# Kernel tuning notes

Hardware: AMD Instinct MI355X
Metric: run time of the kernel (lower is better)

## Reference

```python
import jax, jax.numpy as jnp
import numpy as np

N, K = 10000, 16
EDGE_DIM, HID = 32, 64
MULT = 8            # rep1.mult == rep2.mult (out_mult)
NL = 2              # lvals [0,1] -> 2 irreps per rep
DIM = 4             # (2*0+1) + (2*1+1)
NHEADS = 4
OUT3 = 3 * MULT     # qkv multiplicity
RW_FLAT = NL * NL * MULT * OUT3   # 768 radial-weight outputs per edge
HEAD_DIM = (MULT * DIM) // NHEADS # 8
INDICES = jnp.array([0, 1, 1, 1]) # irrep index for each of the DIM slots (l=0 then l=1 x3)


def setup_inputs() -> dict:
    key = jax.random.key(0)
    ks = jax.random.split(key, 10)
    rn = lambda i, shape, sc=1.0: (jax.random.normal(ks[i], shape, jnp.float32) * sc)
    return {
        "b1": rn(0, (N, K, DIM, NL)),
        "b2": rn(1, (N, K, NL, DIM)),
        "edge_feats": rn(2, (N, K, EDGE_DIM)),
        "f": rn(3, (N, MULT, DIM)),
        "neighbor_idx": jax.random.randint(ks[4], (N, K), 0, N),
        # RadialWeight MLP params (xavier-ish scales, zero biases as in _init_weights)
        "W1": rn(5, (HID, EDGE_DIM), (2.0 / (HID + EDGE_DIM)) ** 0.5),
        "b1_lin": jnp.zeros((HID,), jnp.float32),
        "W2": rn(6, (RW_FLAT, HID), (2.0 / (RW_FLAT + HID)) ** 0.5),
        "b2_lin": jnp.zeros((RW_FLAT,), jnp.float32),
        # EquivariantLinear out_proj params
        "W_out": rn(7, (NL * MULT, MULT), (2.0 / (NL * MULT + MULT)) ** 0.5),
        "bias_out": jnp.zeros((MULT, 1), jnp.float32),
    }


def reference(b1, b2, edge_feats, f, neighbor_idx, W1, b1_lin, W2, b2_lin, W_out, bias_out):
    E = N * K
    b1f = b1.reshape(E, DIM, NL)
    b2f = b2.reshape(E, NL, DIM)
    ef = edge_feats.reshape(E, EDGE_DIM)

    # RadialWeight: 2-layer MLP with exact GELU -> per-edge tensor-product weights
    h = jax.nn.gelu(ef @ W1.T + b1_lin, approximate=False)          # (E, HID)
    rw = (h @ W2.T + b2_lin).reshape(E, NL * OUT3, NL * MULT)        # (E, 48, 16)

    # EquivariantConvolution: gather src node features, chained small matmuls
    f_src = f[neighbor_idx.reshape(-1)]                              # (E, MULT, DIM)
    tmp = jnp.einsum('emd,edl->eml', f_src, b1f)                     # (E, MULT, NL)
    tmp = jnp.matmul(rw, tmp.reshape(E, NL * MULT, 1))               # (E, NL*OUT3, 1)
    qkv = jnp.matmul(tmp.reshape(E, OUT3, NL), b2f)                  # (E, OUT3, DIM)

    # split into q,k,v heads
    qkv = qkv.reshape(N, K, 3 * MULT, DIM)
    q, k_, v = jnp.split(qkv, 3, axis=2)                             # each (N, K, MULT, DIM)
    qh = q.reshape(N, K, NHEADS, HEAD_DIM)
    kh = k_.reshape(N, K, NHEADS, HEAD_DIM)
    vh = v.reshape(N, K, NHEADS, HEAD_DIM)

    # per-edge attention, softmax over the k neighbors
    scale = HEAD_DIM ** -0.5
    scores = jnp.einsum('nkhd,nkhd->nkh', qh, kh) * scale            # (N, K, NHEADS)
    attn = jax.nn.softmax(scores, axis=1)
    out = jnp.einsum('nkh,nkhd->nhd', attn, vh).reshape(N, MULT, DIM)

    # EquivariantLinear out_proj: per-irrep mixing over multiplicity channels
    o = jnp.einsum('om,nmd->nod', W_out, out).reshape(N, NL, MULT, DIM)
    idx = jnp.broadcast_to(INDICES[None, None, None, :], (N, 1, MULT, DIM))
    o = jnp.take_along_axis(o, idx, axis=1)[:, 0]                    # (N, MULT, DIM)
    # bias only on the scalar (l=0) slot; activation is Identity in out_proj
    o = o.at[:, :, 0].add(bias_out[:, 0])
    return o
```

## Files before the change

### kernel.cpp

```cpp
#include <hip/hip_runtime.h>
#include <math.h>

#define E_TOT   160000
#define THREADS 128
#define NBLK    (E_TOT / THREADS)
#define WREG    20480
#define TV_OFF  16384
#define T2S     52

typedef __attribute__((ext_vector_type(8))) __bf16 bf16x8;
typedef __attribute__((ext_vector_type(4))) float f32x4;

static __device__ __forceinline__ unsigned short f2bf(float v) {
    unsigned int u = __float_as_uint(v);
    u += 0x7FFFu + ((u >> 16) & 1u);
    return (unsigned short)(u >> 16);
}
static __device__ __forceinline__ float bf2f(unsigned int s) {
    return __uint_as_float(s << 16);
}

__global__ __launch_bounds__(256) void w2_split(
    const float* __restrict__ W2, uint4* __restrict__ hi4, uint4* __restrict__ lo4)
{
    const int c    = blockIdx.x * 256 + threadIdx.x;
    const int lane = c & 63, rest = c >> 6;
    const int kk   = rest & 1, tj = rest >> 1;
    const int j    = tj & 15,  t  = tj >> 4;
    const int grp  = lane >> 4, r16 = lane & 15;
    const float* src = W2 + (size_t)((t * 16 + r16) * 16 + j) * 64 + kk * 32 + grp * 8;
    union { uint4 u; unsigned short s[8]; } H, L;
    #pragma unroll
    for (int i = 0; i < 8; ++i) {
        float w = src[i];
        unsigned short h = f2bf(w);
        H.s[i] = h;
        L.s[i] = f2bf(w - bf2f(h));
    }
    hi4[c] = H.u;
    lo4[c] = L.u;
}

__global__ __launch_bounds__(THREADS) void eq_attn_kernel(
    const float* __restrict__ b1,
    const float* __restrict__ b2,
    const float* __restrict__ ef,
    const float* __restrict__ f,
    const int*   __restrict__ nidx,
    const float* __restrict__ W1,
    const float* __restrict__ b1l,
    const float* __restrict__ b2l,
    const float* __restrict__ Wout,
    const float* __restrict__ bias,
    const uint4* __restrict__ wsh,
    const uint4* __restrict__ wsl,
    float* __restrict__ out)
{
    __shared__ unsigned char smem[2 * WREG];
    const int tid  = threadIdx.x;
    const int e    = blockIdx.x * THREADS + tid;
    const int wave = tid >> 6;
    const int el   = tid & 63;
    unsigned char* wreg = smem + wave * WREG;

    float efr[32];
    {
        const float4* ef4 = reinterpret_cast<const float4*>(ef + (size_t)e * 32);
        #pragma unroll
        for (int i = 0; i < 8; ++i) {
            float4 v = ef4[i];
            efr[i*4+0] = v.x; efr[i*4+1] = v.y; efr[i*4+2] = v.z; efr[i*4+3] = v.w;
        }
    }
    {
        float h[64];
        #pragma unroll
        for (int hid = 0; hid < 64; ++hid) {
            float acc = b1l[hid];
            #pragma unroll
            for (int c = 0; c < 32; ++c)
                acc = fmaf(efr[c], W1[hid * 32 + c], acc);
            h[hid] = 0.5f * acc * (1.0f + erff(acc * 0.70710678118654752f));
        }
        #pragma unroll
        for (int c8 = 0; c8 < 8; ++c8) {
            union { uint4 u; unsigned short s[8]; } H, L;
            #pragma unroll
            for (int i = 0; i < 8; ++i) {
                float v = h[c8 * 8 + i];
                unsigned short hs = f2bf(v);
                H.s[i] = hs;
                L.s[i] = f2bf(v - bf2f(hs));
            }
            const int ch = c8 ^ (el & 7);
            *(uint4*)(wreg +        el * 128 + ch * 16) = H.u;
            *(uint4*)(wreg + 8192 + el * 128 + ch * 16) = L.u;
        }
    }
    float tmpv[16];
    {
        const int src = nidx[e];
        float fs[32];
        const float4* f4 = reinterpret_cast<const float4*>(f + (size_t)src * 32);
        #pragma unroll
        for (int i = 0; i < 8; ++i) {
            float4 v = f4[i];
            fs[i*4+0] = v.x; fs[i*4+1] = v.y; fs[i*4+2] = v.z; fs[i*4+3] = v.w;
        }
        float b1r[8];
        const float4* b14 = reinterpret_cast<const float4*>(b1 + (size_t)e * 8);
        float4 u0 = b14[0], u1 = b14[1];
        b1r[0]=u0.x; b1r[1]=u0.y; b1r[2]=u0.z; b1r[3]=u0.w;
        b1r[4]=u1.x; b1r[5]=u1.y; b1r[6]=u1.z; b1r[7]=u1.w;
        float* tvp = (float*)(wreg + TV_OFF);
        #pragma unroll
        for (int m = 0; m < 8; ++m) {
            float a0 = 0.f, a1 = 0.f;
            #pragma unroll
            for (int d = 0; d < 4; ++d) {
                a0 = fmaf(fs[m*4+d], b1r[d*2+0], a0);
                a1 = fmaf(fs[m*4+d], b1r[d*2+1], a1);
            }
            tmpv[m*2+0] = a0; tmpv[m*2+1] = a1;
            tvp[(m*2+0) * 64 + el] = a0;
            tvp[(m*2+1) * 64 + el] = a1;
        }
    }

    __syncthreads();

    const int r16 = el & 15;
    const int grp = el >> 4;

    bf16x8 Ahi[4][2], Alo[4][2];
    #pragma unroll
    for (int mt = 0; mt < 4; ++mt)
        #pragma unroll
        for (int kk = 0; kk < 2; ++kk) {
            const int row = mt * 16 + r16;
            const int ch  = (kk * 4 + grp) ^ (r16 & 7);
            Ahi[mt][kk] = *(const bf16x8*)(wreg +        row * 128 + ch * 16);
            Alo[mt][kk] = *(const bf16x8*)(wreg + 8192 + row * 128 + ch * 16);
        }

    f32x4 acc[4][3];
    #pragma unroll
    for (int mt = 0; mt < 4; ++mt)
        #pragma unroll
        for (int t = 0; t < 3; ++t)
            acc[mt][t] = (f32x4){0.f, 0.f, 0.f, 0.f};

    const float* tvp = (const float*)(wreg + TV_OFF);
    for (int j = 0; j < 16; ++j) {
        bf16x8 Bhi[3][2], Blo[3][2];
        #pragma unroll
        for (int t = 0; t < 3; ++t)
            #pragma unroll
            for (int kk = 0; kk < 2; ++kk) {
                const int chunk = ((t * 16 + j) * 2 + kk) * 64 + el;
                Bhi[t][kk] = ((const bf16x8*)wsh)[chunk];
                Blo[t][kk] = ((const bf16x8*)wsl)[chunk];
            }
        #pragma unroll
        for (int mt = 0; mt < 4; ++mt) {
            const int eb = mt * 16 + grp * 4;
            const float tv0 = tvp[j * 64 + eb + 0];
            const float tv1 = tvp[j * 64 + eb + 1];
            const float tv2 = tvp[j * 64 + eb + 2];
            const float tv3 = tvp[j * 64 + eb + 3];
            #pragma unroll
            for (int t = 0; t < 3; ++t) {
                f32x4 rw = (f32x4){0.f, 0.f, 0.f, 0.f};
                rw = __builtin_amdgcn_mfma_f32_16x16x32_bf16(Ahi[mt][0], Bhi[t][0], rw, 0, 0, 0);
                rw = __builtin_amdgcn_mfma_f32_16x16x32_bf16(Ahi[mt][1], Bhi[t][1], rw, 0, 0, 0);
                rw = __builtin_amdgcn_mfma_f32_16x16x32_bf16(Alo[mt][0], Bhi[t][0], rw, 0, 0, 0);
                rw = __builtin_amdgcn_mfma_f32_16x16x32_bf16(Alo[mt][1], Bhi[t][1], rw, 0, 0, 0);
                rw = __builtin_amdgcn_mfma_f32_16x16x32_bf16(Ahi[mt][0], Blo[t][0], rw, 0, 0, 0);
                rw = __builtin_amdgcn_mfma_f32_16x16x32_bf16(Ahi[mt][1], Blo[t][1], rw, 0, 0, 0);
                acc[mt][t].x = fmaf(tv0, rw.x, acc[mt][t].x);
                acc[mt][t].y = fmaf(tv1, rw.y, acc[mt][t].y);
                acc[mt][t].z = fmaf(tv2, rw.z, acc[mt][t].z);
                acc[mt][t].w = fmaf(tv3, rw.w, acc[mt][t].w);
            }
        }
    }

    {
        float* t2p = (float*)wreg;
        #pragma unroll
        for (int mt = 0; mt < 4; ++mt) {
            const int eb = mt * 16 + grp * 4;
            #pragma unroll
            for (int t = 0; t < 3; ++t) {
                t2p[(eb + 0) * T2S + t * 16 + r16] = acc[mt][t].x;
                t2p[(eb + 1) * T2S + t * 16 + r16] = acc[mt][t].y;
                t2p[(eb + 2) * T2S + t * 16 + r16] = acc[mt][t].z;
                t2p[(eb + 3) * T2S + t * 16 + r16] = acc[mt][t].w;
            }
        }
    }

    __syncthreads();

    float t2[48];
    {
        const float* t2r = (const float*)wreg + (size_t)el * T2S;
        #pragma unroll
        for (int o2 = 0; o2 < 48; ++o2) t2[o2] = t2r[o2];
    }
    #pragma unroll
    for (int o2 = 0; o2 < 48; ++o2) {
        float bt = t2[o2];
        #pragma unroll
        for (int j = 0; j < 16; ++j)
            bt = fmaf(tmpv[j], b2l[o2 * 16 + j], bt);
        t2[o2] = bt;
    }

    float b2r[8];
    {
        const float4* b24 = reinterpret_cast<const float4*>(b2 + (size_t)e * 8);
        float4 u0 = b24[0], u1 = b24[1];
        b2r[0]=u0.x; b2r[1]=u0.y; b2r[2]=u0.z; b2r[3]=u0.w;
        b2r[4]=u1.x; b2r[5]=u1.y; b2r[6]=u1.z; b2r[7]=u1.w;
    }
    float q[8][4];
    #pragma unroll
    for (int o = 0; o < 8; ++o) {
        float t0 = t2[2*o+0], t1 = t2[2*o+1];
        #pragma unroll
        for (int d = 0; d < 4; ++d)
            q[o][d] = fmaf(t0, b2r[d], t1 * b2r[4+d]);
    }
    float scores[4] = {0.f, 0.f, 0.f, 0.f};
    #pragma unroll
    for (int o = 0; o < 8; ++o) {
        float t0 = t2[16+2*o+0], t1 = t2[16+2*o+1];
        float sacc = 0.f;
        #pragma unroll
        for (int d = 0; d < 4; ++d) {
            float kr = fmaf(t0, b2r[d], t1 * b2r[4+d]);
            sacc = fmaf(q[o][d], kr, sacc);
        }
        scores[o >> 1] += sacc;
    }
    float vv[8][4];
    #pragma unroll
    for (int o = 0; o < 8; ++o) {
        float t0 = t2[32+2*o+0], t1 = t2[32+2*o+1];
        #pragma unroll
        for (int d = 0; d < 4; ++d)
            vv[o][d] = fmaf(t0, b2r[d], t1 * b2r[4+d]);
    }

    float attn[4];
    #pragma unroll
    for (int hh = 0; hh < 4; ++hh) {
        float s = scores[hh] * 0.35355339059327373f;
        float mx = s;
        #pragma unroll
        for (int msk = 8; msk; msk >>= 1)
            mx = fmaxf(mx, __shfl_xor(mx, msk, 16));
        float p = __expf(s - mx);
        float ps = p;
        #pragma unroll
        for (int msk = 8; msk; msk >>= 1)
            ps += __shfl_xor(ps, msk, 16);
        attn[hh] = p / ps;
    }

    float osum[8][4];
    #pragma unroll
    for (int m = 0; m < 8; ++m) {
        float w = attn[m >> 1];
        #pragma unroll
        for (int d = 0; d < 4; ++d) {
            float val = w * vv[m][d];
            #pragma unroll
            for (int msk = 8; msk; msk >>= 1)
                val += __shfl_xor(val, msk, 16);
            osum[m][d] = val;
        }
    }

    if ((tid & 15) == 0) {
        const int n = e >> 4;
        #pragma unroll
        for (int od = 0; od < 8; ++od) {
            #pragma unroll
            for (int d = 0; d < 4; ++d) {
                const int row = (d == 0) ? od : (8 + od);
                float a = (d == 0) ? bias[od] : 0.f;
                #pragma unroll
                for (int m = 0; m < 8; ++m)
                    a = fmaf(Wout[row * 8 + m], osum[m][d], a);
                out[(size_t)n * 32 + od * 4 + d] = a;
            }
        }
    }
}

extern "C" void kernel_launch(void* const* d_in, const int* in_sizes, int n_in,
                              void* d_out, int out_size, void* d_ws, size_t ws_size,
                              hipStream_t stream) {
    const float* b1   = (const float*)d_in[0];
    const float* b2   = (const float*)d_in[1];
    const float* ef   = (const float*)d_in[2];
    const float* f    = (const float*)d_in[3];
    const int*   nidx = (const int*)d_in[4];
    const float* W1   = (const float*)d_in[5];
    const float* b1l  = (const float*)d_in[6];
    const float* W2   = (const float*)d_in[7];
    const float* b2l  = (const float*)d_in[8];
    const float* Wout = (const float*)d_in[9];
    const float* bias = (const float*)d_in[10];
    float* out = (float*)d_out;

    uint4* wsh = (uint4*)d_ws;
    uint4* wsl = wsh + 6144;

    hipLaunchKernelGGL(w2_split, dim3(24), dim3(256), 0, stream, W2, wsh, wsl);
    hipLaunchKernelGGL(eq_attn_kernel, dim3(NBLK), dim3(THREADS), 0, stream,
                       b1, b2, ef, f, nidx, W1, b1l, b2l, Wout, bias,
                       (const uint4*)wsh, (const uint4*)wsl, out);
}
```

Baseline: 225.2 us.

## Shrink blocks to one wave, cut LDS, polynomial GELU, fold radial bias into MFMA

Each block now holds a single 64-thread wave, and the shared buffer shrinks from 40KB to 13KB. The hi and lo bf16 parts of the hidden activations are staged one after the other through the same LDS region, with extra barriers between them. Exact erf is replaced with an Abramowitz-Stegun polynomial built on a fast reciprocal and exp. The b2 bias contribution moves from a 768-FMA scalar loop into an MFMA initialisation of the accumulators, using a bf16 copy of the bias prepared in the setup kernel. This should raise occupancy and cut VALU work, but the bf16 bias path and the approximate erf lose some precision.

After: 193.4 us. -14.1%, faster.

```diff
diff --git a/kernel.cpp b/kernel.cpp
--- a/kernel.cpp
+++ b/kernel.cpp
@@ -2,11 +2,11 @@
 #include <math.h>
 
 #define E_TOT   160000
-#define THREADS 128
-#define NBLK    (E_TOT / THREADS)
-#define WREG    20480
-#define TV_OFF  16384
+#define TPB     64
+#define NBLK    (E_TOT / TPB)
+#define TV_OFF  8192
 #define T2S     52
+#define SMEM_SZ 13312
 
 typedef __attribute__((ext_vector_type(8))) __bf16 bf16x8;
 typedef __attribute__((ext_vector_type(4))) float f32x4;
@@ -20,28 +20,55 @@
     return __uint_as_float(s << 16);
 }
 
-__global__ __launch_bounds__(256) void w2_split(
-    const float* __restrict__ W2, uint4* __restrict__ hi4, uint4* __restrict__ lo4)
+static __device__ __forceinline__ float gelu_exact(float a) {
+    float x = a * 0.70710678118654752f;
+    float s = fabsf(x);
+    float t = __builtin_amdgcn_rcpf(fmaf(0.3275911f, s, 1.0f));
+    float p = fmaf(1.061405429f, t, -1.453152027f);
+    p = fmaf(p, t, 1.421413741f);
+    p = fmaf(p, t, -0.284496736f);
+    p = fmaf(p, t, 0.254829592f);
+    p = p * t;
+    float er = fmaf(-p, __expf(-s * s), 1.0f);
+    er = copysignf(er, x);
+    return 0.5f * a * (1.0f + er);
+}
+
+__global__ __launch_bounds__(256) void w_split(
+    const float* __restrict__ W2, const float* __restrict__ b2l,
+    uint4* __restrict__ hi4, uint4* __restrict__ lo4, uint4* __restrict__ bb4)
 {
-    const int c    = blockIdx.x * 256 + threadIdx.x;
-    const int lane = c & 63, rest = c >> 6;
-    const int kk   = rest & 1, tj = rest >> 1;
-    const int j    = tj & 15,  t  = tj >> 4;
-    const int grp  = lane >> 4, r16 = lane & 15;
-    const float* src = W2 + (size_t)((t * 16 + r16) * 16 + j) * 64 + kk * 32 + grp * 8;
-    union { uint4 u; unsigned short s[8]; } H, L;
-    #pragma unroll
-    for (int i = 0; i < 8; ++i) {
-        float w = src[i];
-        unsigned short h = f2bf(w);
-        H.s[i] = h;
-        L.s[i] = f2bf(w - bf2f(h));
-    }
-    hi4[c] = H.u;
-    lo4[c] = L.u;
-}
-
-__global__ __launch_bounds__(THREADS) void eq_attn_kernel(
+    const int c = blockIdx.x * 256 + threadIdx.x;
+    if (c < 6144) {
+        const int lane = c & 63, rest = c >> 6;
+        const int kk   = rest & 1, tj = rest >> 1;
+        const int j    = tj & 15,  t  = tj >> 4;
+        const int grp  = lane >> 4, r16 = lane & 15;
+        const float* src = W2 + (size_t)((t * 16 + r16) * 16 + j) * 64 + kk * 32 + grp * 8;
+        union { uint4 u; unsigned short s[8]; } H, L;
+        #pragma unroll
+        for (int i = 0; i < 8; ++i) {
+            float w = src[i];
+            unsigned short h = f2bf(w);
+            H.s[i] = h;
+            L.s[i] = f2bf(w - bf2f(h));
+        }
+        hi4[c] = H.u;
+        lo4[c] = L.u;
+    } else if (c < 6144 + 192) {
+        const int cc   = c - 6144;
+        const int lane = cc & 63, t = cc >> 6;
+        const int grp  = lane >> 4, r16 = lane & 15;
+        union { uint4 u; unsigned short s[8]; } B;
+        #pragma unroll
+        for (int i = 0; i < 8; ++i)
+            B.s[i] = (grp < 2) ? f2bf(b2l[(t * 16 + r16) * 16 + grp * 8 + i])
+                               : (unsigned short)0;
+        bb4[cc] = B.u;
+    }
+}
+
+__global__ __launch_bounds__(TPB) void eq_attn_kernel(
     const float* __restrict__ b1,
     const float* __restrict__ b2,
     const float* __restrict__ ef,
@@ -49,19 +76,18 @@
     const int*   __restrict__ nidx,
     const float* __restrict__ W1,
     const float* __restrict__ b1l,
-    const float* __restrict__ b2l,
     const float* __restrict__ Wout,
     const float* __restrict__ bias,
     const uint4* __restrict__ wsh,
     const uint4* __restrict__ wsl,
+    const uint4* __restrict__ bb,
     float* __restrict__ out)
 {
-    __shared__ unsigned char smem[2 * WREG];
-    const int tid  = threadIdx.x;
-    const int e    = blockIdx.x * THREADS + tid;
-    const int wave = tid >> 6;
-    const int el   = tid & 63;
-    unsigned char* wreg = smem + wave * WREG;
+    __shared__ unsigned char smem[SMEM_SZ];
+    const int tid = threadIdx.x;
+    const int e   = blockIdx.x * TPB + tid;
+    const int r16 = tid & 15;
+    const int grp = tid >> 4;
 
     float efr[32];
     {
@@ -72,30 +98,29 @@
             efr[i*4+0] = v.x; efr[i*4+1] = v.y; efr[i*4+2] = v.z; efr[i*4+3] = v.w;
         }
     }
-    {
-        float h[64];
-        #pragma unroll
-        for (int hid = 0; hid < 64; ++hid) {
-            float acc = b1l[hid];
-            #pragma unroll
-            for (int c = 0; c < 32; ++c)
-                acc = fmaf(efr[c], W1[hid * 32 + c], acc);
-            h[hid] = 0.5f * acc * (1.0f + erff(acc * 0.70710678118654752f));
-        }
+    uint4 Hc[8], Lc[8];
+    {
         #pragma unroll
         for (int c8 = 0; c8 < 8; ++c8) {
             union { uint4 u; unsigned short s[8]; } H, L;
             #pragma unroll
             for (int i = 0; i < 8; ++i) {
-                float v = h[c8 * 8 + i];
+                const int hid = c8 * 8 + i;
+                float acc = b1l[hid];
+                #pragma unroll
+                for (int c = 0; c < 32; ++c)
+                    acc = fmaf(efr[c], W1[hid * 32 + c], acc);
+                float v = gelu_exact(acc);
                 unsigned short hs = f2bf(v);
                 H.s[i] = hs;
                 L.s[i] = f2bf(v - bf2f(hs));
             }
-            const int ch = c8 ^ (el & 7);
-            *(uint4*)(wreg +        el * 128 + ch * 16) = H.u;
-            *(uint4*)(wreg + 8192 + el * 128 + ch * 16) = L.u;
-        }
+            Hc[c8] = H.u;
+            Lc[c8] = L.u;
+        }
+        #pragma unroll
+        for (int c8 = 0; c8 < 8; ++c8)
+            *(uint4*)(smem + tid * 128 + ((c8 ^ (tid & 7)) * 16)) = Hc[c8];
     }
     float tmpv[16];
     {
@@ -112,7 +137,7 @@
         float4 u0 = b14[0], u1 = b14[1];
         b1r[0]=u0.x; b1r[1]=u0.y; b1r[2]=u0.z; b1r[3]=u0.w;
         b1r[4]=u1.x; b1r[5]=u1.y; b1r[6]=u1.z; b1r[7]=u1.w;
-        float* tvp = (float*)(wreg + TV_OFF);
+        float* tvp = (float*)(smem + TV_OFF);
         #pragma unroll
         for (int m = 0; m < 8; ++m) {
             float a0 = 0.f, a1 = 0.f;
@@ -122,16 +147,12 @@
                 a1 = fmaf(fs[m*4+d], b1r[d*2+1], a1);
             }
             tmpv[m*2+0] = a0; tmpv[m*2+1] = a1;
-            tvp[(m*2+0) * 64 + el] = a0;
-            tvp[(m*2+1) * 64 + el] = a1;
-        }
-    }
-
-    __syncthreads();
-
-    const int r16 = el & 15;
-    const int grp = el >> 4;
-
+            tvp[(m*2+0) * 64 + tid] = a0;
+            tvp[(m*2+1) * 64 + tid] = a1;
+        }
+    }
+
+    __syncthreads();
     bf16x8 Ahi[4][2], Alo[4][2];
     #pragma unroll
     for (int mt = 0; mt < 4; ++mt)
@@ -139,35 +160,66 @@
         for (int kk = 0; kk < 2; ++kk) {
             const int row = mt * 16 + r16;
             const int ch  = (kk * 4 + grp) ^ (r16 & 7);
-            Ahi[mt][kk] = *(const bf16x8*)(wreg +        row * 128 + ch * 16);
-            Alo[mt][kk] = *(const bf16x8*)(wreg + 8192 + row * 128 + ch * 16);
-        }
+            Ahi[mt][kk] = *(const bf16x8*)(smem + row * 128 + ch * 16);
+        }
+    __syncthreads();
+    #pragma unroll
+    for (int c8 = 0; c8 < 8; ++c8)
+        *(uint4*)(smem + tid * 128 + ((c8 ^ (tid & 7)) * 16)) = Lc[c8];
+    __syncthreads();
+    #pragma unroll
+    for (int mt = 0; mt < 4; ++mt)
+        #pragma unroll
+        for (int kk = 0; kk < 2; ++kk) {
+            const int row = mt * 16 + r16;
+            const int ch  = (kk * 4 + grp) ^ (r16 & 7);
+            Alo[mt][kk] = *(const bf16x8*)(smem + row * 128 + ch * 16);
+        }
+    __syncthreads();
 
     f32x4 acc[4][3];
-    #pragma unroll
-    for (int mt = 0; mt < 4; ++mt)
-        #pragma unroll
-        for (int t = 0; t < 3; ++t)
-            acc[mt][t] = (f32x4){0.f, 0.f, 0.f, 0.f};
-
-    const float* tvp = (const float*)(wreg + TV_OFF);
+    {
+        const float* tvp = (const float*)(smem + TV_OFF);
+        bf16x8 tvb[4];
+        #pragma unroll
+        for (int mt = 0; mt < 4; ++mt) {
+            union { uint4 u; unsigned short s[8]; } P;
+            #pragma unroll
+            for (int i = 0; i < 8; ++i) {
+                float v = (grp < 2) ? tvp[(grp * 8 + i) * 64 + mt * 16 + r16] : 0.0f;
+                P.s[i] = f2bf(v);
+            }
+            tvb[mt] = *(bf16x8*)&P.u;
+        }
+        bf16x8 blb[3];
+        #pragma unroll
+        for (int t = 0; t < 3; ++t) {
+            uint4 u = bb[t * 64 + tid];
+            blb[t] = *(bf16x8*)&u;
+        }
+        #pragma unroll
+        for (int mt = 0; mt < 4; ++mt)
+            #pragma unroll
+            for (int t = 0; t < 3; ++t)
+                acc[mt][t] = __builtin_amdgcn_mfma_f32_16x16x32_bf16(
+                    tvb[mt], blb[t], (f32x4){0.f, 0.f, 0.f, 0.f}, 0, 0, 0);
+    }
+
+    const float4* tv4 = (const float4*)(smem + TV_OFF);
+    #pragma unroll 4
     for (int j = 0; j < 16; ++j) {
         bf16x8 Bhi[3][2], Blo[3][2];
         #pragma unroll
         for (int t = 0; t < 3; ++t)
             #pragma unroll
             for (int kk = 0; kk < 2; ++kk) {
-                const int chunk = ((t * 16 + j) * 2 + kk) * 64 + el;
+                const int chunk = ((t * 16 + j) * 2 + kk) * 64 + tid;
                 Bhi[t][kk] = ((const bf16x8*)wsh)[chunk];
                 Blo[t][kk] = ((const bf16x8*)wsl)[chunk];
             }
         #pragma unroll
         for (int mt = 0; mt < 4; ++mt) {
-            const int eb = mt * 16 + grp * 4;
-            const float tv0 = tvp[j * 64 + eb + 0];
-            const float tv1 = tvp[j * 64 + eb + 1];
-            const float tv2 = tvp[j * 64 + eb + 2];
-            const float tv3 = tvp[j * 64 + eb + 3];
+            float4 tv = tv4[j * 16 + mt * 4 + grp];
             #pragma unroll
             for (int t = 0; t < 3; ++t) {
                 f32x4 rw = (f32x4){0.f, 0.f, 0.f, 0.f};
@@ -177,16 +229,17 @@
                 rw = __builtin_amdgcn_mfma_f32_16x16x32_bf16(Alo[mt][1], Bhi[t][1], rw, 0, 0, 0);
                 rw = __builtin_amdgcn_mfma_f32_16x16x32_bf16(Ahi[mt][0], Blo[t][0], rw, 0, 0, 0);
                 rw = __builtin_amdgcn_mfma_f32_16x16x32_bf16(Ahi[mt][1], Blo[t][1], rw, 0, 0, 0);
-                acc[mt][t].x = fmaf(tv0, rw.x, acc[mt][t].x);
-                acc[mt][t].y = fmaf(tv1, rw.y, acc[mt][t].y);
-                acc[mt][t].z = fmaf(tv2, rw.z, acc[mt][t].z);
-                acc[mt][t].w = fmaf(tv3, rw.w, acc[mt][t].w);
-            }
-        }
-    }
-
-    {
-        float* t2p = (float*)wreg;
+                acc[mt][t].x = fmaf(tv.x, rw.x, acc[mt][t].x);
+                acc[mt][t].y = fmaf(tv.y, rw.y, acc[mt][t].y);
+                acc[mt][t].z = fmaf(tv.z, rw.z, acc[mt][t].z);
+                acc[mt][t].w = fmaf(tv.w, rw.w, acc[mt][t].w);
+            }
+        }
+    }
+
+    __syncthreads();
+    {
+        float* t2p = (float*)smem;
         #pragma unroll
         for (int mt = 0; mt < 4; ++mt) {
             const int eb = mt * 16 + grp * 4;
@@ -199,22 +252,13 @@
             }
         }
     }
-
     __syncthreads();
 
     float t2[48];
     {
-        const float* t2r = (const float*)wreg + (size_t)el * T2S;
+        const float* t2r = (const float*)smem + (size_t)tid * T2S;
         #pragma unroll
         for (int o2 = 0; o2 < 48; ++o2) t2[o2] = t2r[o2];
-    }
-    #pragma unroll
-    for (int o2 = 0; o2 < 48; ++o2) {
-        float bt = t2[o2];
-        #pragma unroll
-        for (int j = 0; j < 16; ++j)
-            bt = fmaf(tmpv[j], b2l[o2 * 16 + j], bt);
-        t2[o2] = bt;
     }
 
     float b2r[8];
@@ -318,9 +362,10 @@
 
     uint4* wsh = (uint4*)d_ws;
     uint4* wsl = wsh + 6144;
-
-    hipLaunchKernelGGL(w2_split, dim3(24), dim3(256), 0, stream, W2, wsh, wsl);
-    hipLaunchKernelGGL(eq_attn_kernel, dim3(NBLK), dim3(THREADS), 0, stream,
-                       b1, b2, ef, f, nidx, W1, b1l, b2l, Wout, bias,
-                       (const uint4*)wsh, (const uint4*)wsl, out);
-}
+    uint4* bb  = wsh + 12288;
+
+    hipLaunchKernelGGL(w_split, dim3(25), dim3(256), 0, stream, W2, b2l, wsh, wsl, bb);
+    hipLaunchKernelGGL(eq_attn_kernel, dim3(NBLK), dim3(TPB), 0, stream,
+                       b1, b2, ef, f, nidx, W1, b1l, Wout, bias,
+                       (const uint4*)wsh, (const uint4*)wsl, (const uint4*)bb, out);
+}
```
